# Kernel optimization log

Hardware: AMD Instinct MI355X
Metric: run time of the kernel (lower is better)

The kernel has to match this reference:

```python
import jax, jax.numpy as jnp
import numpy as np

B, T, D = 1, 2048, 4096
N, K, H = 32, 8, 128
SLOTS = 32768
THETA = 500000.0
NEG_INF = -1e30


def apply_rope(x, positions, theta=THETA):
    # x: [B, heads, T, H]; positions: [T] int32. Llama half-split rotary.
    h = x.shape[-1]
    inv_freq = 1.0 / (theta ** (jnp.arange(0, h, 2, dtype=jnp.float32) / h))  # [H/2]
    ang = positions.astype(jnp.float32)[:, None] * inv_freq[None, :]          # [T, H/2]
    cos, sin = jnp.cos(ang), jnp.sin(ang)
    x1, x2 = x[..., : h // 2], x[..., h // 2 :]
    return jnp.concatenate([x1 * cos - x2 * sin, x2 * cos + x1 * sin], axis=-1).astype(x.dtype)


def setup_inputs() -> dict:
    key = jax.random.key(0)
    ks = jax.random.split(key, 5)
    x = jax.random.normal(ks[0], (B, T, D), jnp.float32)
    wq = jax.random.normal(ks[1], (N, D, H), jnp.float32) * (D ** -0.5)
    wk = jax.random.normal(ks[2], (K, D, H), jnp.float32) * (D ** -0.5)
    wv = jax.random.normal(ks[3], (K, D, H), jnp.float32) * (D ** -0.5)
    wo = jax.random.normal(ks[4], (N, H, D), jnp.float32) * ((N * H) ** -0.5)
    k_cache = jnp.zeros((SLOTS, K, H), jnp.float32)
    v_cache = jnp.zeros((SLOTS, K, H), jnp.float32)
    positions = jnp.arange(T, dtype=jnp.int32)
    write_indices = jnp.arange(T, dtype=jnp.int32)  # paged-cache slot per token, in [0, SLOTS)
    return dict(x=x, wq=wq, wk=wk, wv=wv, wo=wo, k_cache=k_cache, v_cache=v_cache,
                positions=positions, write_indices=write_indices)


def reference(x, wq, wk, wv, wo, k_cache, v_cache, positions, write_indices):
    # QKV projections (per-head einsum, as in the module)
    q = jnp.einsum('btd,ndh->bnth', x, wq)            # [B,N,T,H]
    k = jnp.einsum('btd,kdh->bkth', x, wk)            # [B,K,T,H]
    v = jnp.einsum('btd,kdh->bkth', x, wv)            # [B,K,T,H]
    # RoPE on q and k, then q scaling by head_dim**-0.5 (applied to q as in source)
    q = apply_rope(q, positions) * (H ** -0.5)
    k = apply_rope(k, positions)
    # KV-cache scatter write (B=1): cache layout [slot, kv_head, head_dim]
    k_cache = k_cache.at[write_indices].set(jnp.transpose(k[0], (1, 0, 2)))
    v_cache = v_cache.at[write_indices].set(jnp.transpose(v[0], (1, 0, 2)))
    # Prefill causal GQA attention over the current sequence
    g = N // K
    qg = q.reshape(B, K, g, T, H)
    scores = jnp.einsum('bkgth,bksh->bkgts', qg, k)   # [B,K,G,T,T]
    mask = positions[:, None] >= positions[None, :]   # causal
    scores = jnp.where(mask, scores, NEG_INF)
    p = jax.nn.softmax(scores, axis=-1)
    attn = jnp.einsum('bkgts,bksh->bkgth', p, v).reshape(B, N, T, H)
    o = jnp.einsum('bnth,nhd->btd', attn, wo)         # [B,T,D]
    return k_cache, v_cache, o
```

## Files before the change

kernel.cpp:

```cpp
#include <hip/hip_runtime.h>
#include <stdint.h>

#define T_SEQ   2048
#define D_MODEL 4096
#define NQ      32
#define NKV     8
#define HD      128
#define NSLOTS  32768
#define L2THETA_64 0.29580575976911624f
#define QSCALE_LOG2E 0.12751743126f

typedef __bf16 bf16;
typedef bf16  bf16x8 __attribute__((ext_vector_type(8)));
typedef float f32x4  __attribute__((ext_vector_type(4)));

#define AS1 __attribute__((address_space(1)))
#define AS3 __attribute__((address_space(3)))

__device__ __forceinline__ void async_ld16(const bf16* g, bf16* l) {
  __builtin_amdgcn_global_load_lds((AS1 void*)(uintptr_t)g, (AS3 void*)l, 16, 0, 0);
}

__global__ __launch_bounds__(256) void convert_bf16(const float* __restrict__ src,
                                                    bf16* __restrict__ dst, int n8) {
  int i = blockIdx.x * blockDim.x + threadIdx.x;
  if (i >= n8) return;
  const float4* s = (const float4*)src + (size_t)i * 2;
  float4 a = s[0], b = s[1];
  bf16x8 o;
  o[0]=(bf16)a.x; o[1]=(bf16)a.y; o[2]=(bf16)a.z; o[3]=(bf16)a.w;
  o[4]=(bf16)b.x; o[5]=(bf16)b.y; o[6]=(bf16)b.z; o[7]=(bf16)b.w;
  *((bf16x8*)dst + i) = o;
}

__global__ __launch_bounds__(256) void transpose_w(const float* __restrict__ src,
                                                   bf16* __restrict__ dst,
                                                   int rows, int cols) {
  __shared__ float tile[32][33];
  const int z = blockIdx.z;
  src += (size_t)z * rows * cols;
  dst += (size_t)z * rows * cols;
  const int c0 = blockIdx.x * 32;
  const int r0 = blockIdx.y * 32;
  const int tx = threadIdx.x;
  const int ty = threadIdx.y;
#pragma unroll
  for (int j = 0; j < 32; j += 8)
    tile[ty + j][tx] = src[(size_t)(r0 + ty + j) * cols + c0 + tx];
  __syncthreads();
#pragma unroll
  for (int j = 0; j < 32; j += 8)
    dst[(size_t)(c0 + ty + j) * rows + r0 + tx] = (bf16)tile[tx][ty + j];
}

__global__ __launch_bounds__(256) void transpose_v(const bf16* __restrict__ src,
                                                   bf16* __restrict__ dst) {
  __shared__ bf16 tile[32][33];
  const int z  = blockIdx.z;
  const int h0 = blockIdx.x * 32;
  const int t0 = blockIdx.y * 32;
  const int tx = threadIdx.x;
  const int ty = threadIdx.y;
  const bf16* s = src + (size_t)z * T_SEQ * HD;
  bf16* d       = dst + (size_t)z * T_SEQ * HD;
#pragma unroll
  for (int j = 0; j < 32; j += 8)
    tile[ty + j][tx] = s[(size_t)(t0 + ty + j) * HD + h0 + tx];
  __syncthreads();
#pragma unroll
  for (int j = 0; j < 32; j += 8)
    d[(size_t)(h0 + ty + j) * T_SEQ + t0 + tx] = tile[tx][ty + j];
}

__global__ __launch_bounds__(256) void mark_slots(const int* __restrict__ wind,
                                                  uint32_t* __restrict__ bm) {
  const int tid = threadIdx.x;
  for (int i = tid; i < NSLOTS / 32; i += 256) bm[i] = 0u;
  __syncthreads();
  for (int i = tid; i < T_SEQ; i += 256) {
    const int s = wind[i];
    atomicOr(&bm[s >> 5], 1u << (s & 31));
  }
}

template <int MODE>
__global__ __launch_bounds__(256) void gemm_bt(
    const bf16* __restrict__ A, const bf16* __restrict__ Bt, int Kd,
    bf16* __restrict__ qb, bf16* __restrict__ kb, bf16* __restrict__ vb,
    float* __restrict__ kc_out, float* __restrict__ vc_out,
    const int* __restrict__ positions, const int* __restrict__ wind,
    float* __restrict__ o_out,
    const float* __restrict__ kc_src, const float* __restrict__ vc_src,
    const uint32_t* __restrict__ slotmap) {
  const int tid  = threadIdx.x;

  if (MODE == 1 && blockIdx.y >= (D_MODEL / 128)) {
    const int cb   = (blockIdx.y - D_MODEL / 128) * gridDim.x + blockIdx.x;
    const int nblk = 16 * gridDim.x;
    for (int s = cb; s < NSLOTS; s += nblk) {
      if (slotmap[s >> 5] & (1u << (s & 31))) continue;
      const size_t base = (size_t)s * (NKV * HD);
      f32x4 kv = __builtin_nontemporal_load((const f32x4*)(kc_src + base) + tid);
      f32x4 vv = __builtin_nontemporal_load((const f32x4*)(vc_src + base) + tid);
      __builtin_nontemporal_store(kv, (f32x4*)(kc_out + base) + tid);
      __builtin_nontemporal_store(vv, (f32x4*)(vc_out + base) + tid);
    }
    return;
  }

  __shared__ bf16 As[2][128 * 32];
  __shared__ bf16 Bs[2][128 * 32];
  const int wid  = tid >> 6;
  const int lane = tid & 63;
  const int quad = lane >> 4;
  const int l15  = lane & 15;
  const int m0 = blockIdx.x * 128;
  const int n0 = blockIdx.y * 128;

  const int srow = tid >> 2;
  const int scol = (tid & 3) * 8;
  const bf16* Ag0 = A  + (size_t)(m0 + srow) * Kd + scol;
  const bf16* Ag1 = Ag0 + (size_t)64 * Kd;
  const bf16* Bg0 = Bt + (size_t)(n0 + srow) * Kd + scol;
  const bf16* Bg1 = Bg0 + (size_t)64 * Kd;

  const f32x4 fz = {0.f, 0.f, 0.f, 0.f};
  f32x4 acc[2][8];
#pragma unroll
  for (int mi = 0; mi < 2; ++mi)
#pragma unroll
    for (int ni = 0; ni < 8; ++ni) acc[mi][ni] = fz;

  const int mrow = wid * 32;
  const int nkt = Kd >> 5;

  async_ld16(Ag0,      &As[0][tid * 8]);
  async_ld16(Ag1,      &As[0][(tid + 256) * 8]);
  async_ld16(Bg0,      &Bs[0][tid * 8]);
  async_ld16(Bg1,      &Bs[0][(tid + 256) * 8]);
  async_ld16(Ag0 + 32, &As[1][tid * 8]);
  async_ld16(Ag1 + 32, &As[1][(tid + 256) * 8]);
  async_ld16(Bg0 + 32, &Bs[1][tid * 8]);
  async_ld16(Bg1 + 32, &Bs[1][(tid + 256) * 8]);

  for (int i = 0; i < nkt; ++i) {
    const bf16* Asc = As[i & 1];
    const bf16* Bsc = Bs[i & 1];
    if (i + 1 < nkt) asm volatile("s_waitcnt vmcnt(4)" ::: "memory");
    else             asm volatile("s_waitcnt vmcnt(0)" ::: "memory");
    __builtin_amdgcn_s_barrier();

    bf16x8 af[2], bfr[8];
#pragma unroll
    for (int mi = 0; mi < 2; ++mi)
      af[mi] = *(const bf16x8*)(Asc + (mrow + mi * 16 + l15) * 32 + quad * 8);
#pragma unroll
    for (int ni = 0; ni < 8; ++ni)
      bfr[ni] = *(const bf16x8*)(Bsc + (ni * 16 + l15) * 32 + quad * 8);

    __builtin_amdgcn_s_setprio(1);
#pragma unroll
    for (int mi = 0; mi < 2; ++mi)
#pragma unroll
      for (int ni = 0; ni < 8; ++ni)
        acc[mi][ni] = __builtin_amdgcn_mfma_f32_16x16x32_bf16(af[mi], bfr[ni], acc[mi][ni], 0, 0, 0);
    __builtin_amdgcn_s_setprio(0);

    asm volatile("" ::: "memory");
    __builtin_amdgcn_s_barrier();
    if (i + 2 < nkt) {
      const int k0 = (i + 2) * 32;
      bf16* Ad = (bf16*)As[i & 1];
      bf16* Bd = (bf16*)Bs[i & 1];
      async_ld16(Ag0 + k0, Ad + tid * 8);
      async_ld16(Ag1 + k0, Ad + (tid + 256) * 8);
      async_ld16(Bg0 + k0, Bd + tid * 8);
      async_ld16(Bg1 + k0, Bd + (tid + 256) * 8);
    }
  }

  if (MODE == 1) {
#pragma unroll
    for (int mi = 0; mi < 2; ++mi)
#pragma unroll
      for (int ni = 0; ni < 8; ++ni)
#pragma unroll
        for (int r = 0; r < 4; ++r) {
          int trow = m0 + mrow + mi * 16 + quad * 4 + r;
          o_out[(size_t)trow * D_MODEL + n0 + ni * 16 + l15] = acc[mi][ni][r];
        }
  } else {
    const int head = blockIdx.y;
#pragma unroll
    for (int mi = 0; mi < 2; ++mi) {
#pragma unroll
      for (int r = 0; r < 4; ++r) {
        const int trow = m0 + mrow + mi * 16 + quad * 4 + r;
        const float pos = (float)positions[trow];
        const int slot = (head >= 32) ? wind[trow] : 0;
#pragma unroll
        for (int ni = 0; ni < 4; ++ni) {
          const int h1 = ni * 16 + l15;
          float a1 = acc[mi][ni][r];
          float a2 = acc[mi][ni + 4][r];
          float o1, o2;
          if (head < 40) {
            float ang = pos * exp2f((float)h1 * -L2THETA_64);
            float sn, cs;
            sincosf(ang, &sn, &cs);
            o1 = a1 * cs - a2 * sn;
            o2 = a2 * cs + a1 * sn;
          } else { o1 = a1; o2 = a2; }
          if (head < 32) {
            o1 *= QSCALE_LOG2E; o2 *= QSCALE_LOG2E;
            bf16* qp = qb + ((size_t)head * T_SEQ + trow) * HD + h1;
            qp[0]  = (bf16)o1;
            qp[64] = (bf16)o2;
          } else if (head < 40) {
            const int kvh = head - 32;
            bf16* kp = kb + ((size_t)kvh * T_SEQ + trow) * HD + h1;
            kp[0]  = (bf16)o1;
            kp[64] = (bf16)o2;
            float* cp = kc_out + ((size_t)slot * NKV + kvh) * HD + h1;
            cp[0]  = o1;
            cp[64] = o2;
          } else {
            const int kvh = head - 40;
            bf16* vp = vb + ((size_t)kvh * T_SEQ + trow) * HD + h1;
            vp[0]  = (bf16)o1;
            vp[64] = (bf16)o2;
            float* cp = vc_out + ((size_t)slot * NKV + kvh) * HD + h1;
            cp[0]  = o1;
            cp[64] = o2;
          }
        }
      }
    }
  }
}

__global__ __launch_bounds__(256, 2) void attn_fused(
    const bf16* __restrict__ qb, const bf16* __restrict__ kb,
    const bf16* __restrict__ vt, bf16* __restrict__ attnb) {
  __shared__ bf16 Ks [64 * 128];
  __shared__ bf16 Vts[128 * 64];
  __shared__ bf16 Ps [4 * 32 * 72];
  const int tid  = threadIdx.x;
  const int wid  = tid >> 6;
  const int lane = tid & 63;
  const int quad = lane >> 4;
  const int l15  = lane & 15;
  const int head = blockIdx.y;
  const int kv   = head >> 2;
  int bt = blockIdx.x;
  if (head & 16) bt = (T_SEQ / 128 - 1) - bt;
  const int t0b  = bt * 128;
  const int t0w  = t0b + wid * 32;

  bf16x8 qf[2][4];
#pragma unroll
  for (int mi = 0; mi < 2; ++mi) {
    const bf16* qp = qb + ((size_t)head * T_SEQ + t0w + mi * 16 + l15) * HD + quad * 8;
#pragma unroll
    for (int ck = 0; ck < 4; ++ck) qf[mi][ck] = *(const bf16x8*)(qp + ck * 32);
  }

  const f32x4 fz = {0.f, 0.f, 0.f, 0.f};
  f32x4 oacc[2][8];
#pragma unroll
  for (int mi = 0; mi < 2; ++mi)
#pragma unroll
    for (int ch = 0; ch < 8; ++ch) oacc[mi][ch] = fz;
  float l_acc[8];
#pragma unroll
  for (int i = 0; i < 8; ++i) l_acc[i] = 0.f;

  const bf16* kbase = kb + (size_t)kv * T_SEQ * HD;
  const bf16* vbase = vt + (size_t)kv * HD * T_SEQ;
  bf16* Pw = Ps + wid * (32 * 72);

  const int nkt = 2 * bt + 2;
  for (int kt = 0; kt < nkt; ++kt) {
    const int tk0 = kt * 64;
#pragma unroll
    for (int i = 0; i < 4; ++i) {
      const int g = i * 256 + tid;
      const int k = g >> 4, c = g & 15;
      uint4 val = *(const uint4*)(kbase + (size_t)(tk0 + k) * HD + c * 8);
      *(uint4*)(Ks + k * 128 + ((c ^ (k & 15)) * 8)) = val;
    }
#pragma unroll
    for (int i = 0; i < 4; ++i) {
      const int g = i * 256 + tid;
      const int h = g >> 3, c = g & 7;
      uint4 val = *(const uint4*)(vbase + (size_t)h * T_SEQ + tk0 + c * 8);
      *(uint4*)(Vts + h * 64 + ((c ^ (h & 7)) * 8)) = val;
    }
    __syncthreads();

    f32x4 s[2][4];
#pragma unroll
    for (int mi = 0; mi < 2; ++mi)
#pragma unroll
      for (int n = 0; n < 4; ++n) s[mi][n] = fz;
#pragma unroll
    for (int n = 0; n < 4; ++n) {
      const int krow = n * 16 + l15;
#pragma unroll
      for (int ck = 0; ck < 4; ++ck) {
        const int cc = (ck * 4 + quad) ^ (krow & 15);
        bf16x8 kf = *(const bf16x8*)(Ks + krow * 128 + cc * 8);
#pragma unroll
        for (int mi = 0; mi < 2; ++mi)
          s[mi][n] = __builtin_amdgcn_mfma_f32_16x16x32_bf16(qf[mi][ck], kf, s[mi][n], 0, 0, 0);
      }
    }

    const bool domask = (tk0 + 63) > t0w;
#pragma unroll
    for (int mi = 0; mi < 2; ++mi)
#pragma unroll
      for (int r = 0; r < 4; ++r) {
        const int row = t0w + mi * 16 + quad * 4 + r;
#pragma unroll
        for (int n = 0; n < 4; ++n) {
          float p = __builtin_amdgcn_exp2f(s[mi][n][r]);
          if (domask && (tk0 + n * 16 + l15 > row)) p = 0.f;
          l_acc[mi * 4 + r] += p;
          Pw[(mi * 16 + quad * 4 + r) * 72 + n * 16 + l15] = (bf16)p;
        }
      }
    asm volatile("s_waitcnt lgkmcnt(0)" ::: "memory");

#pragma unroll
    for (int kk = 0; kk < 2; ++kk) {
      bf16x8 pf[2];
#pragma unroll
      for (int mi = 0; mi < 2; ++mi)
        pf[mi] = *(const bf16x8*)(Pw + (mi * 16 + l15) * 72 + kk * 32 + quad * 8);
#pragma unroll
      for (int ch = 0; ch < 8; ++ch) {
        const int h = ch * 16 + l15;
        const int cc = (kk * 4 + quad) ^ (h & 7);
        bf16x8 vf = *(const bf16x8*)(Vts + h * 64 + cc * 8);
#pragma unroll
        for (int mi = 0; mi < 2; ++mi)
          oacc[mi][ch] = __builtin_amdgcn_mfma_f32_16x16x32_bf16(pf[mi], vf, oacc[mi][ch], 0, 0, 0);
      }
    }
    __syncthreads();
  }

#pragma unroll
  for (int i = 0; i < 8; ++i) {
    float v = l_acc[i];
#pragma unroll
    for (int off = 1; off < 16; off <<= 1) v += __shfl_xor(v, off);
    l_acc[i] = 1.0f / v;
  }
#pragma unroll
  for (int mi = 0; mi < 2; ++mi)
#pragma unroll
    for (int r = 0; r < 4; ++r) {
      const int trow = t0w + mi * 16 + quad * 4 + r;
      const float inv = l_acc[mi * 4 + r];
#pragma unroll
      for (int ch = 0; ch < 8; ++ch)
        attnb[(size_t)trow * D_MODEL + head * HD + ch * 16 + l15] =
            (bf16)(oacc[mi][ch][r] * inv);
    }
}

extern "C" void kernel_launch(void* const* d_in, const int* in_sizes, int n_in,
                              void* d_out, int out_size, void* d_ws, size_t ws_size,
                              hipStream_t stream) {
  (void)in_sizes; (void)n_in; (void)out_size; (void)ws_size;
  const float* x     = (const float*)d_in[0];
  const float* wq    = (const float*)d_in[1];
  const float* wk    = (const float*)d_in[2];
  const float* wv    = (const float*)d_in[3];
  const float* wo    = (const float*)d_in[4];
  const float* kc_in = (const float*)d_in[5];
  const float* vc_in = (const float*)d_in[6];
  const int* positions = (const int*)d_in[7];
  const int* wind      = (const int*)d_in[8];

  float* out    = (float*)d_out;
  float* kc_out = out;
  float* vc_out = out + (size_t)NSLOTS * NKV * HD;
  float* o_out  = out + (size_t)2 * NSLOTS * NKV * HD;

  char* ws = (char*)d_ws;
  bf16* xb     = (bf16*)(ws);
  bf16* wqkv_t = (bf16*)(ws + (16ull  << 20));
  bf16* wo_t   = (bf16*)(ws + (64ull  << 20));
  bf16* qb     = (bf16*)(ws + (96ull  << 20));
  bf16* kb     = (bf16*)(ws + (112ull << 20));
  bf16* vb     = (bf16*)(ws + (116ull << 20));
  bf16* attnb  = xb;
  bf16* vt     = wqkv_t;
  uint32_t* slotmap = (uint32_t*)(ws + (24ull << 20));

  convert_bf16<<<dim3((T_SEQ * D_MODEL / 8 + 255) / 256), dim3(256), 0, stream>>>(
      x, xb, T_SEQ * D_MODEL / 8);
  transpose_w<<<dim3(HD / 32, D_MODEL / 32, NQ),  dim3(32, 8), 0, stream>>>(wq, wqkv_t, D_MODEL, HD);
  transpose_w<<<dim3(HD / 32, D_MODEL / 32, NKV), dim3(32, 8), 0, stream>>>(
      wk, wqkv_t + (size_t)32 * HD * D_MODEL, D_MODEL, HD);
  transpose_w<<<dim3(HD / 32, D_MODEL / 32, NKV), dim3(32, 8), 0, stream>>>(
      wv, wqkv_t + (size_t)40 * HD * D_MODEL, D_MODEL, HD);
  transpose_w<<<dim3(D_MODEL / 32, (NQ * HD) / 32, 1), dim3(32, 8), 0, stream>>>(
      wo, wo_t, NQ * HD, D_MODEL);

  gemm_bt<0><<<dim3(T_SEQ / 128, 48), dim3(256), 0, stream>>>(
      xb, wqkv_t, D_MODEL, qb, kb, vb, kc_out, vc_out, positions, wind, nullptr,
      nullptr, nullptr, nullptr);
  mark_slots<<<dim3(1), dim3(256), 0, stream>>>(wind, slotmap);
  transpose_v<<<dim3(HD / 32, T_SEQ / 32, NKV), dim3(32, 8), 0, stream>>>(vb, vt);
  attn_fused<<<dim3(T_SEQ / 128, NQ), dim3(256), 0, stream>>>(qb, kb, vt, attnb);
  gemm_bt<1><<<dim3(T_SEQ / 128, D_MODEL / 128 + 16), dim3(256), 0, stream>>>(
      attnb, wo_t, D_MODEL, nullptr, nullptr, nullptr, kc_out, vc_out,
      nullptr, nullptr, o_out, kc_in, vc_in, slotmap);
}
```

Baseline: 912.0 us.

## Move KV-cache passthrough copy from output GEMM into attention kernel

```diff
diff --git a/kernel.cpp b/kernel.cpp
--- a/kernel.cpp
+++ b/kernel.cpp
@@ -89,24 +89,8 @@
     bf16* __restrict__ qb, bf16* __restrict__ kb, bf16* __restrict__ vb,
     float* __restrict__ kc_out, float* __restrict__ vc_out,
     const int* __restrict__ positions, const int* __restrict__ wind,
-    float* __restrict__ o_out,
-    const float* __restrict__ kc_src, const float* __restrict__ vc_src,
-    const uint32_t* __restrict__ slotmap) {
+    float* __restrict__ o_out) {
   const int tid  = threadIdx.x;
-
-  if (MODE == 1 && blockIdx.y >= (D_MODEL / 128)) {
-    const int cb   = (blockIdx.y - D_MODEL / 128) * gridDim.x + blockIdx.x;
-    const int nblk = 16 * gridDim.x;
-    for (int s = cb; s < NSLOTS; s += nblk) {
-      if (slotmap[s >> 5] & (1u << (s & 31))) continue;
-      const size_t base = (size_t)s * (NKV * HD);
-      f32x4 kv = __builtin_nontemporal_load((const f32x4*)(kc_src + base) + tid);
-      f32x4 vv = __builtin_nontemporal_load((const f32x4*)(vc_src + base) + tid);
-      __builtin_nontemporal_store(kv, (f32x4*)(kc_out + base) + tid);
-      __builtin_nontemporal_store(vv, (f32x4*)(vc_out + base) + tid);
-    }
-    return;
-  }
 
   __shared__ bf16 As[2][128 * 32];
   __shared__ bf16 Bs[2][128 * 32];
@@ -241,16 +225,48 @@
 
 __global__ __launch_bounds__(256, 2) void attn_fused(
     const bf16* __restrict__ qb, const bf16* __restrict__ kb,
-    const bf16* __restrict__ vt, bf16* __restrict__ attnb) {
+    const bf16* __restrict__ vt, bf16* __restrict__ attnb,
+    const float* __restrict__ kc_src, const float* __restrict__ vc_src,
+    float* __restrict__ kc_out, float* __restrict__ vc_out,
+    const uint32_t* __restrict__ slotmap) {
+  const int tid  = threadIdx.x;
+
+  if (blockIdx.y < 4) {
+    const int cb = blockIdx.y * 16 + blockIdx.x;
+    for (int s0 = cb; s0 < NSLOTS; s0 += 64 * 4) {
+      f32x4 kvv[4][2];
+      bool cp[4];
+#pragma unroll
+      for (int j = 0; j < 4; ++j) {
+        const int s = s0 + 64 * j;
+        cp[j] = !(slotmap[s >> 5] & (1u << (s & 31)));
+        if (cp[j]) {
+          const size_t base = (size_t)s * (NKV * HD);
+          kvv[j][0] = __builtin_nontemporal_load((const f32x4*)(kc_src + base) + tid);
+          kvv[j][1] = __builtin_nontemporal_load((const f32x4*)(vc_src + base) + tid);
+        }
+      }
+#pragma unroll
+      for (int j = 0; j < 4; ++j) {
+        if (cp[j]) {
+          const int s = s0 + 64 * j;
+          const size_t base = (size_t)s * (NKV * HD);
+          __builtin_nontemporal_store(kvv[j][0], (f32x4*)(kc_out + base) + tid);
+          __builtin_nontemporal_store(kvv[j][1], (f32x4*)(vc_out + base) + tid);
+        }
+      }
+    }
+    return;
+  }
+
   __shared__ bf16 Ks [64 * 128];
   __shared__ bf16 Vts[128 * 64];
   __shared__ bf16 Ps [4 * 32 * 72];
-  const int tid  = threadIdx.x;
   const int wid  = tid >> 6;
   const int lane = tid & 63;
   const int quad = lane >> 4;
   const int l15  = lane & 15;
-  const int head = blockIdx.y;
+  const int head = blockIdx.y - 4;
   const int kv   = head >> 2;
   int bt = blockIdx.x;
   if (head & 16) bt = (T_SEQ / 128 - 1) - bt;
@@ -412,12 +428,12 @@
       wo, wo_t, NQ * HD, D_MODEL);
 
   gemm_bt<0><<<dim3(T_SEQ / 128, 48), dim3(256), 0, stream>>>(
-      xb, wqkv_t, D_MODEL, qb, kb, vb, kc_out, vc_out, positions, wind, nullptr,
-      nullptr, nullptr, nullptr);
+      xb, wqkv_t, D_MODEL, qb, kb, vb, kc_out, vc_out, positions, wind, nullptr);
   mark_slots<<<dim3(1), dim3(256), 0, stream>>>(wind, slotmap);
   transpose_v<<<dim3(HD / 32, T_SEQ / 32, NKV), dim3(32, 8), 0, stream>>>(vb, vt);
-  attn_fused<<<dim3(T_SEQ / 128, NQ), dim3(256), 0, stream>>>(qb, kb, vt, attnb);
-  gemm_bt<1><<<dim3(T_SEQ / 128, D_MODEL / 128 + 16), dim3(256), 0, stream>>>(
-      attnb, wo_t, D_MODEL, nullptr, nullptr, nullptr, kc_out, vc_out,
-      nullptr, nullptr, o_out, kc_in, vc_in, slotmap);
-}
+  attn_fused<<<dim3(T_SEQ / 128, 4 + NQ), dim3(256), 0, stream>>>(
+      qb, kb, vt, attnb, kc_in, vc_in, kc_out, vc_out, slotmap);
+  gemm_bt<1><<<dim3(T_SEQ / 128, D_MODEL / 128), dim3(256), 0, stream>>>(
+      attnb, wo_t, D_MODEL, nullptr, nullptr, nullptr, nullptr, nullptr,
+      nullptr, nullptr, o_out);
+}
```

Result: slower. 973.6 us (+6.7%).
